# Kernel tuning notes

Hardware: AMD Instinct MI355X
Metric: run time of the kernel (lower is better)

## Reference

```python
import jax, jax.numpy as jnp
import numpy as np

N = 50000
E = 800000
T = 10
H = 128
D = 64
P = 65536


def setup_inputs() -> dict:
    key = jax.random.key(0)
    ks = jax.random.split(key, 16)
    inp = {}
    inp["node_type_ids"] = jax.random.randint(ks[0], (N,), 0, T)
    inp["adj_rows"] = jax.random.randint(ks[1], (E,), 0, N)
    inp["adj_cols"] = jax.random.randint(ks[2], (E,), 0, N)
    inp["adj_vals"] = jax.random.uniform(ks[3], (E,), dtype=jnp.float32)
    inp["pairs"] = jax.random.randint(ks[4], (2, P), 0, N)
    s = 0.02
    inp["node_emb"] = jax.random.normal(ks[5], (N, H), dtype=jnp.float32) * s
    inp["type_emb"] = jax.random.normal(ks[6], (T, H), dtype=jnp.float32) * s
    inp["W1"] = jax.random.normal(ks[7], (H, H), dtype=jnp.float32) * s
    inp["b1"] = jnp.zeros((H,), dtype=jnp.float32)
    inp["W2"] = jax.random.normal(ks[8], (H, D), dtype=jnp.float32) * s
    inp["b2"] = jnp.zeros((D,), dtype=jnp.float32)
    inp["Wp1"] = jax.random.normal(ks[9], (3 * D, D), dtype=jnp.float32) * s
    inp["bp1"] = jnp.zeros((D,), dtype=jnp.float32)
    inp["Wp2"] = jax.random.normal(ks[10], (D, 1), dtype=jnp.float32) * s
    inp["bp2"] = jnp.zeros((1,), dtype=jnp.float32)
    return inp


def _spmm(rows, cols, vals, x):
    # sparse.mm(adj, x): out[r] = sum_e vals[e] * x[cols[e]] for rows[e]==r
    msgs = vals[:, None] * x[cols]          # [E, F] gather (irregular)
    return jax.ops.segment_sum(msgs, rows, num_segments=N)


def reference(node_type_ids, adj_rows, adj_cols, adj_vals, pairs,
              node_emb, type_emb, W1, b1, W2, b2, Wp1, bp1, Wp2, bp2):
    # encode: node_embedding(arange(N)) is just the full table
    x = node_emb + type_emb[node_type_ids]                    # [N, H]
    h = jax.nn.relu(_spmm(adj_rows, adj_cols, adj_vals, x) @ W1 + b1)  # gcn1 + relu
    # dropout is identity in eval mode
    z = _spmm(adj_rows, adj_cols, adj_vals, h) @ W2 + b2      # [N, D] gcn2
    # score
    src = z[pairs[0]]                                         # [P, D]
    dst = z[pairs[1]]                                         # [P, D]
    feat = jnp.concatenate([src, dst, src * dst], axis=-1)    # [P, 3D]
    out = jax.nn.relu(feat @ Wp1 + bp1) @ Wp2 + bp2           # [P, 1]
    return out[:, 0]
```

## Files before the change

### kernel.cpp

```cpp
#include <hip/hip_runtime.h>

#define N_NODES 50000
#define N_EDGES 800000
#define NPAIRS  65536

#define NBUCK 391
#define RTILE 2048
#define RBLOCKS 391

typedef unsigned short ushort_t;
typedef unsigned int uint_t;
typedef unsigned long long u64_t;
typedef ushort_t ushort8v __attribute__((ext_vector_type(8)));
typedef short bf16x8 __attribute__((ext_vector_type(8)));
typedef float f32x4 __attribute__((ext_vector_type(4)));

__device__ inline ushort_t f2bf(float f) {
    uint_t u = __float_as_uint(f);
    u = (u + 0x7FFF + ((u >> 16) & 1)) >> 16;
    return (ushort_t)u;
}
__device__ inline float bf2f(ushort_t b) {
    return __uint_as_float(((uint_t)b) << 16);
}


__global__ __launch_bounds__(256) void pack_hist_kernel(const int* __restrict__ rows,
                                                        const int* __restrict__ cols,
                                                        const float* __restrict__ vals,
                                                        u64_t* __restrict__ tmpA,
                                                        int* __restrict__ blockhist, int e) {
    __shared__ int lh[NBUCK];
    int blk = blockIdx.x, t = threadIdx.x;
    for (int i = t; i < NBUCK; i += 256) lh[i] = 0;
    __syncthreads();
    int base = blk * RTILE;
#pragma unroll
    for (int k = 0; k < RTILE / 256; k++) {
        int idx = base + k * 256 + t;
        if (idx < e) {
            int r = rows[idx];
            uint_t payload = (uint_t)cols[idx] | ((uint_t)f2bf(vals[idx]) << 16);
            tmpA[idx] = ((u64_t)r << 32) | payload;
            atomicAdd(&lh[r >> 7], 1);
        }
    }
    __syncthreads();
    for (int d = t; d < NBUCK; d += 256) blockhist[d * RBLOCKS + blk] = lh[d];
}

__global__ __launch_bounds__(256) void scan_block_kernel(const int* __restrict__ cnt,
                                                         int* __restrict__ excl,
                                                         int* __restrict__ blksum, int n) {
    __shared__ int s[256];
    int tid = threadIdx.x;
    int i = blockIdx.x * 256 + tid;
    int v = (i < n) ? cnt[i] : 0;
    s[tid] = v; __syncthreads();
    for (int off = 1; off < 256; off <<= 1) {
        int t = (tid >= off) ? s[tid - off] : 0;
        __syncthreads();
        s[tid] += t;
        __syncthreads();
    }
    if (i < n) excl[i] = s[tid] - v;
    if (tid == 255) blksum[blockIdx.x] = s[255];
}

__global__ __launch_bounds__(256) void scan_mid_kernel(int* __restrict__ data, int n) {
    __shared__ int s[256];
    __shared__ int carry;
    int t = threadIdx.x;
    if (t == 0) carry = 0;
    __syncthreads();
    for (int base = 0; base < n; base += 256) {
        int i = base + t;
        int v = (i < n) ? data[i] : 0;
        s[t] = v; __syncthreads();
        for (int off = 1; off < 256; off <<= 1) {
            int x = (t >= off) ? s[t - off] : 0;
            __syncthreads();
            s[t] += x;
            __syncthreads();
        }
        int excl = s[t] - v + carry;
        if (i < n) data[i] = excl;
        __syncthreads();
        if (t == 255) carry += s[255];
        __syncthreads();
    }
}

__global__ __launch_bounds__(256) void scan_add2_kernel(int* __restrict__ data,
                                                        const int* __restrict__ blksum, int n) {
    int i = blockIdx.x * 256 + threadIdx.x;
    if (i < n) data[i] += blksum[blockIdx.x];
}

__global__ __launch_bounds__(256) void radix_scatter_kernel(const u64_t* __restrict__ tmpA,
                                                            const int* __restrict__ gofs,
                                                            u64_t* __restrict__ tmpB, int e) {
    __shared__ u64_t stage[RTILE];
    __shared__ int lh[NBUCK];
    __shared__ int lstart[NBUCK];
    __shared__ int lcur[NBUCK];
    int blk = blockIdx.x, t = threadIdx.x;
    for (int i = t; i < NBUCK; i += 256) lh[i] = 0;
    __syncthreads();
    int base = blk * RTILE;
    int cnt = min(RTILE, e - base);
    for (int k = t; k < cnt; k += 256) {
        int d = (int)(tmpA[base + k] >> 39);
        atomicAdd(&lh[d], 1);
    }
    __syncthreads();
    if (t == 0) {
        int s = 0;
        for (int d = 0; d < NBUCK; d++) { lstart[d] = s; s += lh[d]; }
    }
    __syncthreads();
    for (int i = t; i < NBUCK; i += 256) lcur[i] = lstart[i];
    __syncthreads();
    for (int k = t; k < cnt; k += 256) {
        u64_t it = tmpA[base + k];
        int d = (int)(it >> 39);
        int slot = atomicAdd(&lcur[d], 1);
        stage[slot] = it;
    }
    __syncthreads();
    for (int k = t; k < cnt; k += 256) {
        u64_t it = stage[k];
        int d = (int)(it >> 39);
        tmpB[gofs[d * RBLOCKS + blk] + (k - lstart[d])] = it;
    }
}

__global__ __launch_bounds__(256) void bucket_sort_kernel(const u64_t* __restrict__ tmpB,
                                                          const int* __restrict__ gofs,
                                                          uint_t* __restrict__ csr_edge,
                                                          int* __restrict__ row_ptr, int e, int n) {
    __shared__ uint_t stage[4096];
    __shared__ int lh[128];
    __shared__ int lstart[128];
    __shared__ int lcur[128];
    int d = blockIdx.x, t = threadIdx.x;
    int bstart = gofs[d * RBLOCKS];
    int bend = (d == NBUCK - 1) ? e : gofs[(d + 1) * RBLOCKS];
    int len = bend - bstart;
    for (int i = t; i < 128; i += 256) lh[i] = 0;
    __syncthreads();
    for (int k = t; k < len; k += 256) {
        int lr = (int)((tmpB[bstart + k] >> 32) & 127);
        atomicAdd(&lh[lr], 1);
    }
    __syncthreads();
    if (t == 0) {
        int s = 0;
        for (int j = 0; j < 128; j++) { lstart[j] = s; s += lh[j]; }
    }
    __syncthreads();
    if (t < 128) {
        int grow = d * 128 + t;
        if (grow <= n) row_ptr[grow] = bstart + lstart[t];
    }
    for (int i = t; i < 128; i += 256) lcur[i] = lstart[i];
    __syncthreads();
    for (int k = t; k < len; k += 256) {
        u64_t it = tmpB[bstart + k];
        int lr = (int)((it >> 32) & 127);
        int slot = atomicAdd(&lcur[lr], 1);
        stage[slot] = (uint_t)it;
    }
    __syncthreads();
    for (int k = t; k < len; k += 256) csr_edge[bstart + k] = stage[k];
}


__global__ __launch_bounds__(256) void prep_w_kernel(const float* __restrict__ W1,
                                                     const float* __restrict__ W2,
                                                     ushort_t* __restrict__ Wt1,
                                                     ushort_t* __restrict__ Wt2) {
    int g = blockIdx.x * 256 + threadIdx.x;
    if (g < 2048) {
        int c = g & 127, k8 = g >> 7;
        ushort8v o;
#pragma unroll
        for (int j = 0; j < 8; j++) o[j] = f2bf(W1[(size_t)(k8 * 8 + j) * 128 + c]);
        *(ushort8v*)&Wt1[(size_t)c * 128 + k8 * 8] = o;
    } else if (g < 3072) {
        int g2 = g - 2048;
        int c = g2 & 63, k8 = g2 >> 6;
        ushort8v o;
#pragma unroll
        for (int j = 0; j < 8; j++) o[j] = f2bf(W2[(size_t)(k8 * 8 + j) * 64 + c]);
        *(ushort8v*)&Wt2[(size_t)c * 128 + k8 * 8] = o;
    }
}


__global__ __launch_bounds__(256) void gemm1_mfma_kernel(const float* __restrict__ node_emb,
                                                         const float* __restrict__ type_emb,
                                                         const int* __restrict__ tids,
                                                         const ushort_t* __restrict__ Wt1,
                                                         ushort_t* __restrict__ y, int n) {
    __shared__ __align__(16) ushort_t As[64 * 128];
    __shared__ __align__(16) ushort_t Ws[128 * 128];
    int t = threadIdx.x;

    for (int gi = t; gi < 2048; gi += 256) {
        int c = gi >> 4, kg = gi & 15;
        ushort8v v = *(const ushort8v*)&Wt1[gi * 8];
        *(ushort8v*)&Ws[c * 128 + ((kg ^ (c & 7)) << 3)] = v;
    }
    int row_l = t >> 2;
    int row_g = blockIdx.x * 64 + row_l;
    int kseg = (t & 3) * 32;
    if (row_g < n) {
        int tv = tids[row_g];
        const float4* na = (const float4*)(node_emb + (size_t)row_g * 128 + kseg);
        const float4* ta = (const float4*)(type_emb + (size_t)tv * 128 + kseg);
#pragma unroll
        for (int i2 = 0; i2 < 4; i2++) {
            float4 a = na[i2 * 2], b = ta[i2 * 2];
            float4 a2 = na[i2 * 2 + 1], b2 = ta[i2 * 2 + 1];
            ushort8v o;
            o[0] = f2bf(a.x + b.x);  o[1] = f2bf(a.y + b.y);
            o[2] = f2bf(a.z + b.z);  o[3] = f2bf(a.w + b.w);
            o[4] = f2bf(a2.x + b2.x); o[5] = f2bf(a2.y + b2.y);
            o[6] = f2bf(a2.z + b2.z); o[7] = f2bf(a2.w + b2.w);
            int kg = (t & 3) * 4 + i2;
            *(ushort8v*)&As[row_l * 128 + ((kg ^ (row_l & 7)) << 3)] = o;
        }
    } else {
        ushort8v z = (ushort8v)(ushort_t)0;
#pragma unroll
        for (int i2 = 0; i2 < 4; i2++) {
            int kg = (t & 3) * 4 + i2;
            *(ushort8v*)&As[row_l * 128 + ((kg ^ (row_l & 7)) << 3)] = z;
        }
    }
    __syncthreads();

    int lane = t & 63, wid = t >> 6;
    int m0 = (wid & 1) * 32, n0 = (wid >> 1) * 64;
    int lr = lane & 15, lk = lane >> 4;
    f32x4 acc[2][4] = {};
#pragma unroll
    for (int ks = 0; ks < 4; ks++) {
        int kg = ks * 4 + lk;
        bf16x8 afr[2];
#pragma unroll
        for (int mt = 0; mt < 2; mt++) {
            int r = m0 + mt * 16 + lr;
            afr[mt] = *(const bf16x8*)&As[r * 128 + ((kg ^ (r & 7)) << 3)];
        }
#pragma unroll
        for (int nt = 0; nt < 4; nt++) {
            int c = n0 + nt * 16 + lr;
            bf16x8 bfr = *(const bf16x8*)&Ws[c * 128 + ((kg ^ (c & 7)) << 3)];
            acc[0][nt] = __builtin_amdgcn_mfma_f32_16x16x32_bf16(afr[0], bfr, acc[0][nt], 0, 0, 0);
            acc[1][nt] = __builtin_amdgcn_mfma_f32_16x16x32_bf16(afr[1], bfr, acc[1][nt], 0, 0, 0);
        }
    }
#pragma unroll
    for (int mt = 0; mt < 2; mt++) {
#pragma unroll
        for (int j = 0; j < 4; j++) {
            int rg = blockIdx.x * 64 + m0 + mt * 16 + lk * 4 + j;
            if (rg < n) {
#pragma unroll
                for (int nt = 0; nt < 4; nt++) {
                    int c = n0 + nt * 16 + lr;
                    y[(size_t)rg * 128 + c] = f2bf(acc[mt][nt][j]);
                }
            }
        }
    }
}


__global__ __launch_bounds__(256) void gemm2_mfma_kernel(const ushort_t* __restrict__ h,
                                                         const ushort_t* __restrict__ Wt2,
                                                         ushort_t* __restrict__ g, int n) {
    __shared__ __align__(16) ushort_t As[64 * 128];
    __shared__ __align__(16) ushort_t Ws[64 * 128];
    int t = threadIdx.x;

    for (int gi = t; gi < 1024; gi += 256) {
        int c = gi >> 4, kg = gi & 15;
        ushort8v v = *(const ushort8v*)&Wt2[gi * 8];
        *(ushort8v*)&Ws[c * 128 + ((kg ^ (c & 7)) << 3)] = v;
    }
    int row_l = t >> 2;
    int row_g = blockIdx.x * 64 + row_l;
    int kseg = (t & 3) * 32;
    if (row_g < n) {
        const ushort8v* hr = (const ushort8v*)(h + (size_t)row_g * 128 + kseg);
#pragma unroll
        for (int i2 = 0; i2 < 4; i2++) {
            ushort8v v = hr[i2];
            int kg = (t & 3) * 4 + i2;
            *(ushort8v*)&As[row_l * 128 + ((kg ^ (row_l & 7)) << 3)] = v;
        }
    } else {
        ushort8v z = (ushort8v)(ushort_t)0;
#pragma unroll
        for (int i2 = 0; i2 < 4; i2++) {
            int kg = (t & 3) * 4 + i2;
            *(ushort8v*)&As[row_l * 128 + ((kg ^ (row_l & 7)) << 3)] = z;
        }
    }
    __syncthreads();

    int lane = t & 63, wid = t >> 6;
    int m0 = (wid & 1) * 32, n0 = (wid >> 1) * 32;
    int lr = lane & 15, lk = lane >> 4;
    f32x4 acc[2][2] = {};
#pragma unroll
    for (int ks = 0; ks < 4; ks++) {
        int kg = ks * 4 + lk;
        bf16x8 afr[2];
#pragma unroll
        for (int mt = 0; mt < 2; mt++) {
            int r = m0 + mt * 16 + lr;
            afr[mt] = *(const bf16x8*)&As[r * 128 + ((kg ^ (r & 7)) << 3)];
        }
#pragma unroll
        for (int nt = 0; nt < 2; nt++) {
            int c = n0 + nt * 16 + lr;
            bf16x8 bfr = *(const bf16x8*)&Ws[c * 128 + ((kg ^ (c & 7)) << 3)];
            acc[0][nt] = __builtin_amdgcn_mfma_f32_16x16x32_bf16(afr[0], bfr, acc[0][nt], 0, 0, 0);
            acc[1][nt] = __builtin_amdgcn_mfma_f32_16x16x32_bf16(afr[1], bfr, acc[1][nt], 0, 0, 0);
        }
    }
#pragma unroll
    for (int mt = 0; mt < 2; mt++) {
#pragma unroll
        for (int j = 0; j < 4; j++) {
            int rg = blockIdx.x * 64 + m0 + mt * 16 + lk * 4 + j;
            if (rg < n) {
#pragma unroll
                for (int nt = 0; nt < 2; nt++) {
                    int c = n0 + nt * 16 + lr;
                    g[(size_t)rg * 64 + c] = f2bf(acc[mt][nt][j]);
                }
            }
        }
    }
}


template <int F, bool RELU, bool BF16OUT>
__global__ __launch_bounds__(256) void spmm_v3_kernel(const int* __restrict__ row_ptr,
                                                      const uint_t* __restrict__ csr_edge,
                                                      const ushort_t* __restrict__ src,
                                                      const float* __restrict__ bias,
                                                      void* __restrict__ dst) {
    constexpr int CGN = F / 8;
    constexpr int EGN = 64 / CGN;
    int wid = threadIdx.x >> 6, lane = threadIdx.x & 63;
    int row = blockIdx.x * 4 + wid;
    if (row >= N_NODES) return;
    int eg = lane / CGN;
    int c8 = (lane % CGN) * 8;
    int start = row_ptr[row], end = row_ptr[row + 1];

    float acc[8] = {};
    for (int base = start; base < end; base += 64) {
        int idx = base + lane;
        uint_t pe = 0;
        if (idx < end) pe = csr_edge[idx];
        int cnt = min(64, end - base);
        int jmax = (cnt + EGN - 1) / EGN;
        for (int j = 0; j < jmax; j++) {
            int el = j * EGN + eg;
            uint_t p = (uint_t)__shfl((int)pe, el);
            if (el < cnt) {
                int cc = p & 0xFFFF;
                float vv = bf2f((ushort_t)(p >> 16));
                const ushort8v s = *(const ushort8v*)(src + (size_t)cc * F + c8);
#pragma unroll
                for (int m = 0; m < 8; m++) acc[m] += vv * bf2f(s[m]);
            }
        }
    }
#pragma unroll
    for (int off = CGN; off < 64; off <<= 1) {
#pragma unroll
        for (int m = 0; m < 8; m++) acc[m] += __shfl_xor(acc[m], off);
    }
    if (eg == 0) {
#pragma unroll
        for (int m = 0; m < 8; m++) {
            acc[m] += bias[c8 + m];
            if (RELU) acc[m] = fmaxf(acc[m], 0.f);
        }
        if (BF16OUT) {
            ushort8v o;
#pragma unroll
            for (int m = 0; m < 8; m++) o[m] = f2bf(acc[m]);
            *(ushort8v*)((ushort_t*)dst + (size_t)row * F + c8) = o;
        } else {
            float4 o0 = make_float4(acc[0], acc[1], acc[2], acc[3]);
            float4 o1 = make_float4(acc[4], acc[5], acc[6], acc[7]);
            *(float4*)((float*)dst + (size_t)row * F + c8) = o0;
            *(float4*)((float*)dst + (size_t)row * F + c8 + 4) = o1;
        }
    }
}


__global__ __launch_bounds__(256) void pair_kernel(const int* __restrict__ pairs,
                                                   const float* __restrict__ z,
                                                   const float* __restrict__ Wp1,
                                                   const float* __restrict__ bp1,
                                                   const float* __restrict__ Wp2,
                                                   const float* __restrict__ bp2,
                                                   float* __restrict__ out) {
    __shared__ float As[32][33];
    __shared__ float Ws[32][64];
    int t = threadIdx.x;
    int tx = t & 15, ty = t >> 4;
    int row0 = blockIdx.x * 32;
    const int* p0s = pairs;
    const int* p1s = pairs + NPAIRS;
    float acc[2][4] = {};
    int lrow = t >> 3, lk0 = (t & 7) << 2;
    int rg = row0 + lrow;
    int p0 = p0s[rg], p1 = p1s[rg];
    for (int kc = 0; kc < 192; kc += 32) {
        float4 v;
        if (kc < 64) {
            v = *(const float4*)(z + (size_t)p0 * 64 + kc + lk0);
        } else if (kc < 128) {
            v = *(const float4*)(z + (size_t)p1 * 64 + (kc - 64) + lk0);
        } else {
            float4 a = *(const float4*)(z + (size_t)p0 * 64 + (kc - 128) + lk0);
            float4 b = *(const float4*)(z + (size_t)p1 * 64 + (kc - 128) + lk0);
            v = make_float4(a.x * b.x, a.y * b.y, a.z * b.z, a.w * b.w);
        }
        As[lrow][lk0 + 0] = v.x; As[lrow][lk0 + 1] = v.y;
        As[lrow][lk0 + 2] = v.z; As[lrow][lk0 + 3] = v.w;
#pragma unroll
        for (int l = 0; l < 2; l++) {
            int idx = l * 1024 + t * 4;
            int kk = idx >> 6, c = idx & 63;
            *(float4*)&Ws[kk][c] = *(const float4*)(Wp1 + (size_t)(kc + kk) * 64 + c);
        }
        __syncthreads();
#pragma unroll
        for (int kk = 0; kk < 32; kk++) {
            float4 w = *(const float4*)&Ws[kk][tx * 4];
#pragma unroll
            for (int i = 0; i < 2; i++) {
                float a = As[ty + 16 * i][kk];
                acc[i][0] += a * w.x; acc[i][1] += a * w.y;
                acc[i][2] += a * w.z; acc[i][3] += a * w.w;
            }
        }
        __syncthreads();
    }
    float b0 = bp1[tx * 4], b1v = bp1[tx * 4 + 1], b2v = bp1[tx * 4 + 2], b3v = bp1[tx * 4 + 3];
    float w0 = Wp2[tx * 4], w1 = Wp2[tx * 4 + 1], w2 = Wp2[tx * 4 + 2], w3 = Wp2[tx * 4 + 3];
#pragma unroll
    for (int i = 0; i < 2; i++) {
        float p = fmaxf(acc[i][0] + b0, 0.f) * w0 + fmaxf(acc[i][1] + b1v, 0.f) * w1 +
                  fmaxf(acc[i][2] + b2v, 0.f) * w2 + fmaxf(acc[i][3] + b3v, 0.f) * w3;
        p += __shfl_xor(p, 1);
        p += __shfl_xor(p, 2);
        p += __shfl_xor(p, 4);
        p += __shfl_xor(p, 8);
        if (tx == 0) out[row0 + ty + 16 * i] = p + bp2[0];
    }
}


extern "C" void kernel_launch(void* const* d_in, const int* in_sizes, int n_in,
                              void* d_out, int out_size, void* d_ws, size_t ws_size,
                              hipStream_t stream) {
    const int*   tids     = (const int*)d_in[0];
    const int*   adj_rows = (const int*)d_in[1];
    const int*   adj_cols = (const int*)d_in[2];
    const float* adj_vals = (const float*)d_in[3];
    const int*   pairs    = (const int*)d_in[4];
    const float* node_emb = (const float*)d_in[5];
    const float* type_emb = (const float*)d_in[6];
    const float* W1  = (const float*)d_in[7];
    const float* b1  = (const float*)d_in[8];
    const float* W2  = (const float*)d_in[9];
    const float* b2  = (const float*)d_in[10];
    const float* Wp1 = (const float*)d_in[11];
    const float* bp1 = (const float*)d_in[12];
    const float* Wp2 = (const float*)d_in[13];
    const float* bp2 = (const float*)d_in[14];
    float* out = (float*)d_out;

    int n = in_sizes[0];
    int e = in_sizes[1];
    int p = in_sizes[4] / 2;

    char* ws = (char*)d_ws;
    ushort_t* bufY = (ushort_t*)ws;
    u64_t* tmpA = (u64_t*)ws;
    char* wsB = ws + (size_t)n * 128 * sizeof(ushort_t);
    ushort_t* bufH = (ushort_t*)wsB;
    float* bufZ = (float*)wsB;
    u64_t* tmpB = (u64_t*)wsB;

    int* row_ptr   = (int*)(wsB + (size_t)n * 128 * sizeof(ushort_t));
    int* blockhist = row_ptr + (n + 1);
    int L  = NBUCK * RBLOCKS;
    int* blksum1   = blockhist + L;
    uint_t* csr_edge = (uint_t*)(blksum1 + 1024);
    ushort_t* Wt1 = (ushort_t*)(csr_edge + e);
    ushort_t* Wt2 = Wt1 + 128 * 128;

    int SG = (L + 255) / 256;

    prep_w_kernel<<<12, 256, 0, stream>>>(W1, W2, Wt1, Wt2);
    pack_hist_kernel<<<RBLOCKS, 256, 0, stream>>>(adj_rows, adj_cols, adj_vals, tmpA, blockhist, e);
    scan_block_kernel<<<SG, 256, 0, stream>>>(blockhist, blockhist, blksum1, L);
    scan_mid_kernel<<<1, 256, 0, stream>>>(blksum1, SG);
    scan_add2_kernel<<<SG, 256, 0, stream>>>(blockhist, blksum1, L);
    radix_scatter_kernel<<<RBLOCKS, 256, 0, stream>>>(tmpA, blockhist, tmpB, e);
    bucket_sort_kernel<<<NBUCK, 256, 0, stream>>>(tmpB, blockhist, csr_edge, row_ptr, e, n);

    int rgrid = (n + 3) / 4;
    gemm1_mfma_kernel<<<(n + 63) / 64, 256, 0, stream>>>(node_emb, type_emb, tids, Wt1, bufY, n);
    spmm_v3_kernel<128, true, true><<<rgrid, 256, 0, stream>>>(row_ptr, csr_edge, bufY, b1, bufH);
    gemm2_mfma_kernel<<<(n + 63) / 64, 256, 0, stream>>>(bufH, Wt2, bufY, n);
    spmm_v3_kernel<64, false, false><<<rgrid, 256, 0, stream>>>(row_ptr, csr_edge, bufY, b2, bufZ);
    pair_kernel<<<p / 32, 256, 0, stream>>>(pairs, bufZ, Wp1, bp1, Wp2, bp2, out);
}
```

Baseline: 155.8 us.

## Store SpMM feature matrices in 32-column chunked layout and split SpMM by chunk

New measurement: 213.1 us. 1.37x slower.

```diff
diff --git a/kernel.cpp b/kernel.cpp
--- a/kernel.cpp
+++ b/kernel.cpp
@@ -271,7 +271,7 @@
 #pragma unroll
                 for (int nt = 0; nt < 4; nt++) {
                     int c = n0 + nt * 16 + lr;
-                    y[(size_t)rg * 128 + c] = f2bf(acc[mt][nt][j]);
+                    y[((size_t)(c >> 5) * n + rg) * 32 + (c & 31)] = f2bf(acc[mt][nt][j]);
                 }
             }
         }
@@ -293,20 +293,20 @@
     }
     int row_l = t >> 2;
     int row_g = blockIdx.x * 64 + row_l;
-    int kseg = (t & 3) * 32;
+    int ch = t & 3;
     if (row_g < n) {
-        const ushort8v* hr = (const ushort8v*)(h + (size_t)row_g * 128 + kseg);
+        const ushort8v* hr = (const ushort8v*)(h + ((size_t)ch * n + row_g) * 32);
 #pragma unroll
         for (int i2 = 0; i2 < 4; i2++) {
             ushort8v v = hr[i2];
-            int kg = (t & 3) * 4 + i2;
+            int kg = ch * 4 + i2;
             *(ushort8v*)&As[row_l * 128 + ((kg ^ (row_l & 7)) << 3)] = v;
         }
     } else {
         ushort8v z = (ushort8v)(ushort_t)0;
 #pragma unroll
         for (int i2 = 0; i2 < 4; i2++) {
-            int kg = (t & 3) * 4 + i2;
+            int kg = ch * 4 + i2;
             *(ushort8v*)&As[row_l * 128 + ((kg ^ (row_l & 7)) << 3)] = z;
         }
     }
@@ -342,7 +342,7 @@
 #pragma unroll
                 for (int nt = 0; nt < 2; nt++) {
                     int c = n0 + nt * 16 + lr;
-                    g[(size_t)rg * 64 + c] = f2bf(acc[mt][nt][j]);
+                    g[((size_t)(c >> 5) * n + rg) * 32 + (c & 31)] = f2bf(acc[mt][nt][j]);
                 }
             }
         }
@@ -350,19 +350,21 @@
 }
 
 
-template <int F, bool RELU, bool BF16OUT>
-__global__ __launch_bounds__(256) void spmm_v3_kernel(const int* __restrict__ row_ptr,
+template <int NCHUNK, bool RELU, bool BF16OUT>
+__global__ __launch_bounds__(256) void spmm_ck_kernel(const int* __restrict__ row_ptr,
                                                       const uint_t* __restrict__ csr_edge,
-                                                      const ushort_t* __restrict__ src,
+                                                      const ushort_t* __restrict__ src_base,
                                                       const float* __restrict__ bias,
-                                                      void* __restrict__ dst) {
-    constexpr int CGN = F / 8;
-    constexpr int EGN = 64 / CGN;
+                                                      void* __restrict__ dst, int n) {
+    constexpr int SH = (NCHUNK == 4) ? 2 : 1;
+    int ch = blockIdx.x & (NCHUNK - 1);
+    int rowblk = blockIdx.x >> SH;
     int wid = threadIdx.x >> 6, lane = threadIdx.x & 63;
-    int row = blockIdx.x * 4 + wid;
-    if (row >= N_NODES) return;
-    int eg = lane / CGN;
-    int c8 = (lane % CGN) * 8;
+    int row = rowblk * 4 + wid;
+    if (row >= n) return;
+    const ushort_t* src = src_base + (size_t)ch * n * 32;
+    int eg = lane >> 2;
+    int c8 = (lane & 3) * 8;
     int start = row_ptr[row], end = row_ptr[row + 1];
 
     float acc[8] = {};
@@ -371,40 +373,41 @@
         uint_t pe = 0;
         if (idx < end) pe = csr_edge[idx];
         int cnt = min(64, end - base);
-        int jmax = (cnt + EGN - 1) / EGN;
+        int jmax = (cnt + 15) >> 4;
         for (int j = 0; j < jmax; j++) {
-            int el = j * EGN + eg;
+            int el = j * 16 + eg;
             uint_t p = (uint_t)__shfl((int)pe, el);
             if (el < cnt) {
                 int cc = p & 0xFFFF;
                 float vv = bf2f((ushort_t)(p >> 16));
-                const ushort8v s = *(const ushort8v*)(src + (size_t)cc * F + c8);
+                const ushort8v s = *(const ushort8v*)(src + (size_t)cc * 32 + c8);
 #pragma unroll
                 for (int m = 0; m < 8; m++) acc[m] += vv * bf2f(s[m]);
             }
         }
     }
 #pragma unroll
-    for (int off = CGN; off < 64; off <<= 1) {
+    for (int off = 4; off < 64; off <<= 1) {
 #pragma unroll
         for (int m = 0; m < 8; m++) acc[m] += __shfl_xor(acc[m], off);
     }
     if (eg == 0) {
+        int cg = ch * 32 + c8;
 #pragma unroll
         for (int m = 0; m < 8; m++) {
-            acc[m] += bias[c8 + m];
+            acc[m] += bias[cg + m];
             if (RELU) acc[m] = fmaxf(acc[m], 0.f);
         }
         if (BF16OUT) {
             ushort8v o;
 #pragma unroll
             for (int m = 0; m < 8; m++) o[m] = f2bf(acc[m]);
-            *(ushort8v*)((ushort_t*)dst + (size_t)row * F + c8) = o;
+            *(ushort8v*)((ushort_t*)dst + ((size_t)ch * n + row) * 32 + c8) = o;
         } else {
             float4 o0 = make_float4(acc[0], acc[1], acc[2], acc[3]);
             float4 o1 = make_float4(acc[4], acc[5], acc[6], acc[7]);
-            *(float4*)((float*)dst + (size_t)row * F + c8) = o0;
-            *(float4*)((float*)dst + (size_t)row * F + c8 + 4) = o1;
+            *(float4*)((float*)dst + (size_t)row * (NCHUNK * 32) + cg) = o0;
+            *(float4*)((float*)dst + (size_t)row * (NCHUNK * 32) + cg + 4) = o1;
         }
     }
 }
@@ -527,8 +530,8 @@
 
     int rgrid = (n + 3) / 4;
     gemm1_mfma_kernel<<<(n + 63) / 64, 256, 0, stream>>>(node_emb, type_emb, tids, Wt1, bufY, n);
-    spmm_v3_kernel<128, true, true><<<rgrid, 256, 0, stream>>>(row_ptr, csr_edge, bufY, b1, bufH);
+    spmm_ck_kernel<4, true, true><<<rgrid * 4, 256, 0, stream>>>(row_ptr, csr_edge, bufY, b1, bufH, n);
     gemm2_mfma_kernel<<<(n + 63) / 64, 256, 0, stream>>>(bufH, Wt2, bufY, n);
-    spmm_v3_kernel<64, false, false><<<rgrid, 256, 0, stream>>>(row_ptr, csr_edge, bufY, b2, bufZ);
+    spmm_ck_kernel<2, false, false><<<rgrid * 2, 256, 0, stream>>>(row_ptr, csr_edge, bufY, b2, bufZ, n);
     pair_kernel<<<p / 32, 256, 0, stream>>>(pairs, bufZ, Wp1, bp1, Wp2, bp2, out);
 }
```

## Map one row per lane-group in SpMM instead of one row per wavefront

Applied to the files above, without the earlier changes.

After: 151.7 us, median of 2. 1.03x faster.

```diff
diff --git a/kernel.cpp b/kernel.cpp
--- a/kernel.cpp
+++ b/kernel.cpp
@@ -351,61 +351,51 @@
 
 
 template <int F, bool RELU, bool BF16OUT>
-__global__ __launch_bounds__(256) void spmm_v3_kernel(const int* __restrict__ row_ptr,
+__global__ __launch_bounds__(256) void spmm_v4_kernel(const int* __restrict__ row_ptr,
                                                       const uint_t* __restrict__ csr_edge,
                                                       const ushort_t* __restrict__ src,
                                                       const float* __restrict__ bias,
-                                                      void* __restrict__ dst) {
-    constexpr int CGN = F / 8;
-    constexpr int EGN = 64 / CGN;
-    int wid = threadIdx.x >> 6, lane = threadIdx.x & 63;
-    int row = blockIdx.x * 4 + wid;
-    if (row >= N_NODES) return;
-    int eg = lane / CGN;
-    int c8 = (lane % CGN) * 8;
+                                                      void* __restrict__ dst, int n) {
+    constexpr int GL = F / 8;
+    constexpr int RPB = (64 / GL) * 4;
+    int t = threadIdx.x;
+    int lane = t & 63, wid = t >> 6;
+    int gl = lane % GL;
+    int gbase = lane - gl;
+    int row = blockIdx.x * RPB + wid * (64 / GL) + (lane / GL);
+    int c8 = gl * 8;
+    if (row >= n) return;
     int start = row_ptr[row], end = row_ptr[row + 1];
 
     float acc[8] = {};
-    for (int base = start; base < end; base += 64) {
-        int idx = base + lane;
-        uint_t pe = 0;
-        if (idx < end) pe = csr_edge[idx];
-        int cnt = min(64, end - base);
-        int jmax = (cnt + EGN - 1) / EGN;
-        for (int j = 0; j < jmax; j++) {
-            int el = j * EGN + eg;
-            uint_t p = (uint_t)__shfl((int)pe, el);
-            if (el < cnt) {
-                int cc = p & 0xFFFF;
-                float vv = bf2f((ushort_t)(p >> 16));
-                const ushort8v s = *(const ushort8v*)(src + (size_t)cc * F + c8);
-#pragma unroll
-                for (int m = 0; m < 8; m++) acc[m] += vv * bf2f(s[m]);
-            }
-        }
-    }
-#pragma unroll
-    for (int off = CGN; off < 64; off <<= 1) {
-#pragma unroll
-        for (int m = 0; m < 8; m++) acc[m] += __shfl_xor(acc[m], off);
-    }
-    if (eg == 0) {
-#pragma unroll
-        for (int m = 0; m < 8; m++) {
-            acc[m] += bias[c8 + m];
-            if (RELU) acc[m] = fmaxf(acc[m], 0.f);
-        }
-        if (BF16OUT) {
-            ushort8v o;
-#pragma unroll
-            for (int m = 0; m < 8; m++) o[m] = f2bf(acc[m]);
-            *(ushort8v*)((ushort_t*)dst + (size_t)row * F + c8) = o;
-        } else {
-            float4 o0 = make_float4(acc[0], acc[1], acc[2], acc[3]);
-            float4 o1 = make_float4(acc[4], acc[5], acc[6], acc[7]);
-            *(float4*)((float*)dst + (size_t)row * F + c8) = o0;
-            *(float4*)((float*)dst + (size_t)row * F + c8 + 4) = o1;
-        }
+    for (int base = start; base < end; base += GL) {
+        int idx = base + gl;
+        uint_t pe = (idx < end) ? csr_edge[idx] : 0u;
+        int cnt = min(GL, end - base);
+        for (int j = 0; j < cnt; j++) {
+            uint_t p = (uint_t)__shfl((int)pe, gbase + j);
+            int cc = p & 0xFFFF;
+            float vv = bf2f((ushort_t)(p >> 16));
+            const ushort8v s = *(const ushort8v*)(src + (size_t)cc * F + c8);
+#pragma unroll
+            for (int m = 0; m < 8; m++) acc[m] += vv * bf2f(s[m]);
+        }
+    }
+#pragma unroll
+    for (int m = 0; m < 8; m++) {
+        acc[m] += bias[c8 + m];
+        if (RELU) acc[m] = fmaxf(acc[m], 0.f);
+    }
+    if (BF16OUT) {
+        ushort8v o;
+#pragma unroll
+        for (int m = 0; m < 8; m++) o[m] = f2bf(acc[m]);
+        *(ushort8v*)((ushort_t*)dst + (size_t)row * F + c8) = o;
+    } else {
+        float4 o0 = make_float4(acc[0], acc[1], acc[2], acc[3]);
+        float4 o1 = make_float4(acc[4], acc[5], acc[6], acc[7]);
+        *(float4*)((float*)dst + (size_t)row * F + c8) = o0;
+        *(float4*)((float*)dst + (size_t)row * F + c8 + 4) = o1;
     }
 }
 
@@ -525,10 +515,9 @@
     radix_scatter_kernel<<<RBLOCKS, 256, 0, stream>>>(tmpA, blockhist, tmpB, e);
     bucket_sort_kernel<<<NBUCK, 256, 0, stream>>>(tmpB, blockhist, csr_edge, row_ptr, e, n);
 
-    int rgrid = (n + 3) / 4;
     gemm1_mfma_kernel<<<(n + 63) / 64, 256, 0, stream>>>(node_emb, type_emb, tids, Wt1, bufY, n);
-    spmm_v3_kernel<128, true, true><<<rgrid, 256, 0, stream>>>(row_ptr, csr_edge, bufY, b1, bufH);
+    spmm_v4_kernel<128, true, true><<<(n + 15) / 16, 256, 0, stream>>>(row_ptr, csr_edge, bufY, b1, bufH, n);
     gemm2_mfma_kernel<<<(n + 63) / 64, 256, 0, stream>>>(bufH, Wt2, bufY, n);
-    spmm_v3_kernel<64, false, false><<<rgrid, 256, 0, stream>>>(row_ptr, csr_edge, bufY, b2, bufZ);
+    spmm_v4_kernel<64, false, false><<<(n + 31) / 32, 256, 0, stream>>>(row_ptr, csr_edge, bufY, b2, bufZ, n);
     pair_kernel<<<p / 32, 256, 0, stream>>>(pairs, bufZ, Wp1, bp1, Wp2, bp2, out);
 }
```
